# Optimization experiments

Hardware: AMD Instinct MI355X
Metric: run time of the kernel (lower is better)

Reference implementation:

```python
import jax, jax.numpy as jnp
import numpy as np

SCALE = 30.0
MARGIN = 0.4
H = 0.333
NUM_CLASSES = 100000
EMB = 512
BATCH = 512


def setup_inputs() -> dict:
    key = jax.random.key(0)
    k1, k2, k3 = jax.random.split(key, 3)
    embeddings = jax.random.normal(k1, (BATCH, EMB), dtype=jnp.float32)
    labels = jax.random.randint(k2, (BATCH,), 0, NUM_CLASSES, dtype=jnp.int64)
    # xavier_uniform: bound = sqrt(6 / (fan_in + fan_out)) with fan_in=EMB, fan_out=NUM_CLASSES
    bound = float(np.sqrt(6.0 / (EMB + NUM_CLASSES)))
    weight = jax.random.uniform(k3, (NUM_CLASSES, EMB), dtype=jnp.float32, minval=-bound, maxval=bound)
    return {"embeddings": embeddings, "labels": labels, "weight": weight}


def reference(embeddings, labels, weight):
    n = embeddings.shape[0]
    rows = jnp.arange(n)

    emb_norm = jnp.linalg.norm(embeddings, axis=1, keepdims=True)      # [N,1]
    w_unit = weight / jnp.linalg.norm(weight, axis=1, keepdims=True)   # [C,D]
    emb_unit = embeddings / emb_norm                                   # [N,D]
    cosine = emb_unit @ w_unit.T                                       # [N,C]

    batch_mean = jnp.mean(emb_norm)
    batch_std = jnp.std(emb_norm, ddof=1)  # torch.std is unbiased
    margin_scaler = jnp.clip((emb_norm - batch_mean) / (batch_std + H), -1.0, 1.0)  # [N,1]
    adaptive_margin = MARGIN * (1.0 + margin_scaler[:, 0])             # [N]

    # Apply angular margin only at the label position (equivalent to the
    # one_hot scatter + where in the original, without a second N x C pass).
    cos_t = cosine[rows, labels]                                       # [N]
    cos_t_m = jnp.cos(jnp.arccos(cos_t) + adaptive_margin)             # [N]
    logits = SCALE * cosine.at[rows, labels].set(cos_t_m)              # [N,C]

    # cross-entropy with mean reduction
    lse = jax.nn.logsumexp(logits, axis=1)                             # [N]
    loss = jnp.mean(lse - logits[rows, labels])
    return loss
```

## Files before the change

kernel.cpp:

```cpp
#include <hip/hip_runtime.h>
#include <hip/hip_bf16.h>

#define C_NUM 100000
#define D_EMB 512
#define N_BATCH 512
#define SCALE_F 30.0f
#define MARGIN_F 0.4f
#define H_F 0.333f
#define NT2 782
#define NCH 16

typedef __attribute__((ext_vector_type(8))) short bf16x8;
typedef __attribute__((ext_vector_type(4))) short bf16x4;
typedef __attribute__((ext_vector_type(4))) float f32x4;
typedef __attribute__((ext_vector_type(16))) float f32x16;

static __device__ __forceinline__ short f2bf(float f) {
  __hip_bfloat16 h = __float2bfloat16(f);
  union { __hip_bfloat16 b; short s; } u;
  u.b = h;
  return u.s;
}

static __device__ __forceinline__ float sq4(f32x4 v) {
  return v[0]*v[0] + v[1]*v[1] + v[2]*v[2] + v[3]*v[3];
}

static __device__ __forceinline__ void gload16(const void* g, void* l) {
  __builtin_amdgcn_global_load_lds(
      (const __attribute__((address_space(1))) void*)g,
      (__attribute__((address_space(3))) void*)l, 16, 0, 0);
}

__global__ __launch_bounds__(64) void k_rownorm(const float* __restrict__ emb,
                                                short* __restrict__ Aunit,
                                                float* __restrict__ norms) {
  const int i = blockIdx.x;
  const int l = threadIdx.x;
  const f32x4* row = reinterpret_cast<const f32x4*>(emb + (size_t)i * D_EMB);
  f32x4 v0 = row[l];
  f32x4 v1 = row[l + 64];
  float ss = sq4(v0) + sq4(v1);
#pragma unroll
  for (int m = 1; m < 64; m <<= 1) ss += __shfl_xor(ss, m);
  float nrm = sqrtf(ss);
  float inv = 1.0f / nrm;
  bf16x4 o0, o1;
#pragma unroll
  for (int q = 0; q < 4; ++q) { o0[q] = f2bf(v0[q] * inv); o1[q] = f2bf(v1[q] * inv); }
  bf16x4* dst = reinterpret_cast<bf16x4*>(Aunit + (size_t)i * D_EMB);
  dst[l] = o0;
  dst[l + 64] = o1;
  if (l == 0) norms[i] = nrm;
}

__global__ __launch_bounds__(512) void k_stats(const float* __restrict__ norms,
                                               float* __restrict__ marg) {
  __shared__ float red[8];
  const int t = threadIdx.x;
  const int lane = t & 63, wid = t >> 6;
  float x = norms[t];
  float s = x;
#pragma unroll
  for (int m = 1; m < 64; m <<= 1) s += __shfl_xor(s, m);
  if (lane == 0) red[wid] = s;
  __syncthreads();
  float tot = 0.f;
#pragma unroll
  for (int q = 0; q < 8; ++q) tot += red[q];
  const float mean = tot / 512.f;
  __syncthreads();
  float d = x - mean;
  float s2 = d * d;
#pragma unroll
  for (int m = 1; m < 64; m <<= 1) s2 += __shfl_xor(s2, m);
  if (lane == 0) red[wid] = s2;
  __syncthreads();
  float tot2 = 0.f;
#pragma unroll
  for (int q = 0; q < 8; ++q) tot2 += red[q];
  const float stdv = sqrtf(tot2 / 511.f);
  float msc = (x - mean) / (stdv + H_F);
  msc = fminf(1.f, fmaxf(-1.f, msc));
  marg[t] = MARGIN_F * (1.f + msc);
}

__global__ __launch_bounds__(256, 4) void k_main(const short* __restrict__ Aunit,
                                                 const float* __restrict__ weight,
                                                 const int* __restrict__ labels,
                                                 const float* __restrict__ marg,
                                                 float* __restrict__ partial,
                                                 float* __restrict__ tlogit) {
  __shared__ alignas(16) char As[2][8192];
  __shared__ alignas(16) char Ws[2][10240];
  __shared__ float winv[128];

  const int bid = blockIdx.x;
  const int grp = bid >> 5, within = bid & 31;
  const int rt = (within >> 3) & 3;
  const int ct = grp * 8 + (within & 7);
  if (ct >= NT2) return;

  const int tid = threadIdx.x;
  const int w = tid >> 6, lane = tid & 63;
  const int l31 = lane & 31, lhi = lane >> 5;

  const int ar0 = w * 32 + (lane >> 2);
  const int ak0 = ((lane & 3) * 16) ^ (((ar0 >> 1) & 3) << 4);
  const char* gA0 = (const char*)Aunit + (size_t)(rt * 128 + ar0) * 1024 + ak0;
  const char* gA1 = gA0 + (size_t)16 * 1024;

  const int sc8 = tid >> 3;
  const int su  = tid & 7;
  const float* wsrc[4];
  int wdst[4];
#pragma unroll
  for (int r = 0; r < 4; ++r) {
    int cls = r * 32 + sc8;
    int gcl = ct * 128 + cls; if (gcl > C_NUM - 1) gcl = C_NUM - 1;
    wsrc[r] = weight + (size_t)gcl * D_EMB + su * 4;
    wdst[r] = cls * 80 + su * 8;
  }

  const int xa = ((l31 >> 1) & 3) << 4;
  const int abase = (w * 32 + l31) * 64;

  f32x16 acc0, acc1, acc2, acc3;
#pragma unroll
  for (int q = 0; q < 16; ++q) { acc0[q] = 0.f; acc1[q] = 0.f; acc2[q] = 0.f; acc3[q] = 0.f; }
  float ssq0 = 0.f, ssq1 = 0.f, ssq2 = 0.f, ssq3 = 0.f;

  {
    gload16(gA0, &As[0][w * 2048]);
    gload16(gA1, &As[0][w * 2048 + 1024]);
    gA0 += 64; gA1 += 64;
    f32x4 v0 = *(const f32x4*)(wsrc[0]); wsrc[0] += 32;
    f32x4 v1 = *(const f32x4*)(wsrc[1]); wsrc[1] += 32;
    f32x4 v2 = *(const f32x4*)(wsrc[2]); wsrc[2] += 32;
    f32x4 v3 = *(const f32x4*)(wsrc[3]); wsrc[3] += 32;
    ssq0 += sq4(v0); ssq1 += sq4(v1); ssq2 += sq4(v2); ssq3 += sq4(v3);
    bf16x4 p0, p1, p2, p3;
#pragma unroll
    for (int e = 0; e < 4; ++e) { p0[e] = f2bf(v0[e]); p1[e] = f2bf(v1[e]);
                                  p2[e] = f2bf(v2[e]); p3[e] = f2bf(v3[e]); }
    *(bf16x4*)(&Ws[0][wdst[0]]) = p0;
    *(bf16x4*)(&Ws[0][wdst[1]]) = p1;
    *(bf16x4*)(&Ws[0][wdst[2]]) = p2;
    *(bf16x4*)(&Ws[0][wdst[3]]) = p3;
  }
  __syncthreads();

  int cur = 0;
  for (int c = 0; c < NCH; ++c) {
    const bool more = c < NCH - 1;
    f32x4 v0, v1, v2, v3;
    if (more) {
      gload16(gA0, &As[cur ^ 1][w * 2048]);
      gload16(gA1, &As[cur ^ 1][w * 2048 + 1024]);
      gA0 += 64; gA1 += 64;
      v0 = *(const f32x4*)(wsrc[0]); wsrc[0] += 32;
      v1 = *(const f32x4*)(wsrc[1]); wsrc[1] += 32;
      v2 = *(const f32x4*)(wsrc[2]); wsrc[2] += 32;
      v3 = *(const f32x4*)(wsrc[3]); wsrc[3] += 32;
    }

    const char* Ab = As[cur];
    const char* Wb = Ws[cur];
#pragma unroll
    for (int kk = 0; kk < 2; ++kk) {
      const int kb = kk * 32 + lhi * 16;
      bf16x8 a  = *(const bf16x8*)(Ab + abase + (kb ^ xa));
      bf16x8 b0 = *(const bf16x8*)(Wb + (l31)       * 80 + kb);
      bf16x8 b1 = *(const bf16x8*)(Wb + (32  + l31) * 80 + kb);
      bf16x8 b2 = *(const bf16x8*)(Wb + (64  + l31) * 80 + kb);
      bf16x8 b3 = *(const bf16x8*)(Wb + (96  + l31) * 80 + kb);
      acc0 = __builtin_amdgcn_mfma_f32_32x32x16_bf16(a, b0, acc0, 0, 0, 0);
      acc1 = __builtin_amdgcn_mfma_f32_32x32x16_bf16(a, b1, acc1, 0, 0, 0);
      acc2 = __builtin_amdgcn_mfma_f32_32x32x16_bf16(a, b2, acc2, 0, 0, 0);
      acc3 = __builtin_amdgcn_mfma_f32_32x32x16_bf16(a, b3, acc3, 0, 0, 0);
    }

    if (more) {
      ssq0 += sq4(v0); ssq1 += sq4(v1); ssq2 += sq4(v2); ssq3 += sq4(v3);
      bf16x4 p0, p1, p2, p3;
#pragma unroll
      for (int e = 0; e < 4; ++e) { p0[e] = f2bf(v0[e]); p1[e] = f2bf(v1[e]);
                                    p2[e] = f2bf(v2[e]); p3[e] = f2bf(v3[e]); }
      char* nb = (char*)Ws[cur ^ 1];
      *(bf16x4*)(nb + wdst[0]) = p0;
      *(bf16x4*)(nb + wdst[1]) = p1;
      *(bf16x4*)(nb + wdst[2]) = p2;
      *(bf16x4*)(nb + wdst[3]) = p3;
    }
    __syncthreads();
    cur ^= 1;
  }

  {
    float s0 = ssq0, s1 = ssq1, s2 = ssq2, s3 = ssq3;
#pragma unroll
    for (int m = 1; m < 8; m <<= 1) {
      s0 += __shfl_xor(s0, m); s1 += __shfl_xor(s1, m);
      s2 += __shfl_xor(s2, m); s3 += __shfl_xor(s3, m);
    }
    if (su == 0) {
      winv[sc8]      = (s0 > 0.f) ? rsqrtf(s0) : 0.f;
      winv[32 + sc8] = (s1 > 0.f) ? rsqrtf(s1) : 0.f;
      winv[64 + sc8] = (s2 > 0.f) ? rsqrtf(s2) : 0.f;
      winv[96 + sc8] = (s3 > 0.f) ? rsqrtf(s3) : 0.f;
    }
  }
  __syncthreads();

  const float wv0 = winv[l31];
  const float wv1 = winv[32 + l31];
  const float wv2 = winv[64 + l31];
  const float wv3 = winv[96 + l31];
  const int cb = ct * 128;
#pragma unroll
  for (int r = 0; r < 16; ++r) {
    const int rowf = (r & 3) + 8 * (r >> 2) + 4 * lhi;
    const int R = rt * 128 + w * 32 + rowf;
    const int lab = labels[R];
    float v = 0.f;
#pragma unroll
    for (int ni = 0; ni < 4; ++ni) {
      const int gcc = cb + ni * 32 + l31;
      const float wv = (ni == 0) ? wv0 : (ni == 1) ? wv1 : (ni == 2) ? wv2 : wv3;
      const float av = (ni == 0) ? acc0[r] : (ni == 1) ? acc1[r] : (ni == 2) ? acc2[r] : acc3[r];
      const float cosv = av * wv;
      float lg = SCALE_F * cosv;
      if (lab == gcc) {
        float ctv = fminf(1.f, fmaxf(-1.f, cosv));
        float lt = SCALE_F * cosf(acosf(ctv) + marg[R]);
        lg = lt;
        tlogit[R] = lt;
      }
      v += (gcc < C_NUM) ? __expf(lg) : 0.f;
    }
    v += __shfl_xor(v, 1);
    v += __shfl_xor(v, 2);
    v += __shfl_xor(v, 4);
    v += __shfl_xor(v, 8);
    v += __shfl_xor(v, 16);
    if (l31 == 0) partial[(size_t)ct * N_BATCH + R] = v;
  }
}

__global__ __launch_bounds__(64) void k_reduce(const float* __restrict__ partial,
                                               const float* __restrict__ tlogit,
                                               float* __restrict__ term) {
  const int r = blockIdx.x;
  const int l = threadIdx.x;
  float s = 0.f;
  for (int b = l; b < NT2; b += 64)
    s += partial[(size_t)b * N_BATCH + r];
#pragma unroll
  for (int m = 1; m < 64; m <<= 1) s += __shfl_xor(s, m);
  if (l == 0) term[r] = logf(s) - tlogit[r];
}

__global__ __launch_bounds__(512) void k_final(const float* __restrict__ term,
                                               float* __restrict__ out) {
  __shared__ float red[8];
  const int t = threadIdx.x;
  const int lane = t & 63, wid = t >> 6;
  float v = term[t];
#pragma unroll
  for (int m = 1; m < 64; m <<= 1) v += __shfl_xor(v, m);
  if (lane == 0) red[wid] = v;
  __syncthreads();
  if (t == 0) {
    float tot = 0.f;
#pragma unroll
    for (int q = 0; q < 8; ++q) tot += red[q];
    out[0] = tot / 512.f;
  }
}

extern "C" void kernel_launch(void* const* d_in, const int* in_sizes, int n_in,
                              void* d_out, int out_size, void* d_ws, size_t ws_size,
                              hipStream_t stream) {
  const float* emb    = (const float*)d_in[0];
  const int*   labels = (const int*)d_in[1];
  const float* weight = (const float*)d_in[2];
  float* out = (float*)d_out;

  char* ws = (char*)d_ws;
  short* Aunit   = (short*)ws;
  float* norms   = (float*)(ws + 524288);
  float* marg    = (float*)(ws + 524288 + 2048);
  float* tlog    = (float*)(ws + 524288 + 4096);
  float* term    = (float*)(ws + 524288 + 6144);
  float* partial = (float*)(ws + 524288 + 8192);

  k_rownorm<<<N_BATCH, 64, 0, stream>>>(emb, Aunit, norms);
  k_stats<<<1, 512, 0, stream>>>(norms, marg);
  k_main<<<98 * 32, 256, 0, stream>>>(Aunit, weight, labels, marg, partial, tlog);
  k_reduce<<<N_BATCH, 64, 0, stream>>>(partial, tlog, term);
  k_final<<<1, 512, 0, stream>>>(term, out);
}
```

Before: 137.5 us.

## Deepen weight prefetch to two chunks with explicit waitcnt and MFMA priority

Restructures the main GEMM loop into a manually unrolled ping-pong that keeps two chunks of fp32 weight loads in flight in registers, using explicit vmcnt/lgkmcnt waits and sched_barriers in place of compiler-managed scheduling. MFMA sections run at raised wave priority via s_setprio. The goal is to hide global weight-load latency behind the matrix math. The extra prefetch registers lead to lowering launch-bounds occupancy from 4 to 3 blocks per CU, which can reduce latency hiding across waves, and the hand-written waitcnt counts must exactly match the in-flight loads to stay correct.

```diff
diff --git a/kernel.cpp b/kernel.cpp
--- a/kernel.cpp
+++ b/kernel.cpp
@@ -85,7 +85,7 @@
   marg[t] = MARGIN_F * (1.f + msc);
 }
 
-__global__ __launch_bounds__(256, 4) void k_main(const short* __restrict__ Aunit,
+__global__ __launch_bounds__(256, 3) void k_main(const short* __restrict__ Aunit,
                                                  const float* __restrict__ weight,
                                                  const int* __restrict__ labels,
                                                  const float* __restrict__ marg,
@@ -107,19 +107,25 @@
 
   const int ar0 = w * 32 + (lane >> 2);
   const int ak0 = ((lane & 3) * 16) ^ (((ar0 >> 1) & 3) << 4);
-  const char* gA0 = (const char*)Aunit + (size_t)(rt * 128 + ar0) * 1024 + ak0;
-  const char* gA1 = gA0 + (size_t)16 * 1024;
+  const char* gAb0 = (const char*)Aunit + (size_t)(rt * 128 + ar0) * 1024 + ak0;
+  const char* gAb1 = gAb0 + (size_t)16 * 1024;
 
   const int sc8 = tid >> 3;
   const int su  = tid & 7;
-  const float* wsrc[4];
-  int wdst[4];
-#pragma unroll
-  for (int r = 0; r < 4; ++r) {
-    int cls = r * 32 + sc8;
-    int gcl = ct * 128 + cls; if (gcl > C_NUM - 1) gcl = C_NUM - 1;
-    wsrc[r] = weight + (size_t)gcl * D_EMB + su * 4;
-    wdst[r] = cls * 80 + su * 8;
+  const float* wbase0; const float* wbase1; const float* wbase2; const float* wbase3;
+  int wdst0, wdst1, wdst2, wdst3;
+  {
+    int c0 = 0 * 32 + sc8, c1 = 1 * 32 + sc8, c2 = 2 * 32 + sc8, c3 = 3 * 32 + sc8;
+    int g0 = ct * 128 + c0; if (g0 > C_NUM - 1) g0 = C_NUM - 1;
+    int g1 = ct * 128 + c1; if (g1 > C_NUM - 1) g1 = C_NUM - 1;
+    int g2 = ct * 128 + c2; if (g2 > C_NUM - 1) g2 = C_NUM - 1;
+    int g3 = ct * 128 + c3; if (g3 > C_NUM - 1) g3 = C_NUM - 1;
+    wbase0 = weight + (size_t)g0 * D_EMB + su * 4;
+    wbase1 = weight + (size_t)g1 * D_EMB + su * 4;
+    wbase2 = weight + (size_t)g2 * D_EMB + su * 4;
+    wbase3 = weight + (size_t)g3 * D_EMB + su * 4;
+    wdst0 = c0 * 80 + su * 8; wdst1 = c1 * 80 + su * 8;
+    wdst2 = c2 * 80 + su * 8; wdst3 = c3 * 80 + su * 8;
   }
 
   const int xa = ((l31 >> 1) & 3) << 4;
@@ -130,70 +136,90 @@
   for (int q = 0; q < 16; ++q) { acc0[q] = 0.f; acc1[q] = 0.f; acc2[q] = 0.f; acc3[q] = 0.f; }
   float ssq0 = 0.f, ssq1 = 0.f, ssq2 = 0.f, ssq3 = 0.f;
 
-  {
-    gload16(gA0, &As[0][w * 2048]);
-    gload16(gA1, &As[0][w * 2048 + 1024]);
-    gA0 += 64; gA1 += 64;
-    f32x4 v0 = *(const f32x4*)(wsrc[0]); wsrc[0] += 32;
-    f32x4 v1 = *(const f32x4*)(wsrc[1]); wsrc[1] += 32;
-    f32x4 v2 = *(const f32x4*)(wsrc[2]); wsrc[2] += 32;
-    f32x4 v3 = *(const f32x4*)(wsrc[3]); wsrc[3] += 32;
-    ssq0 += sq4(v0); ssq1 += sq4(v1); ssq2 += sq4(v2); ssq3 += sq4(v3);
-    bf16x4 p0, p1, p2, p3;
-#pragma unroll
-    for (int e = 0; e < 4; ++e) { p0[e] = f2bf(v0[e]); p1[e] = f2bf(v1[e]);
-                                  p2[e] = f2bf(v2[e]); p3[e] = f2bf(v3[e]); }
-    *(bf16x4*)(&Ws[0][wdst[0]]) = p0;
-    *(bf16x4*)(&Ws[0][wdst[1]]) = p1;
-    *(bf16x4*)(&Ws[0][wdst[2]]) = p2;
-    *(bf16x4*)(&Ws[0][wdst[3]]) = p3;
-  }
-  __syncthreads();
-
-  int cur = 0;
-  for (int c = 0; c < NCH; ++c) {
-    const bool more = c < NCH - 1;
-    f32x4 v0, v1, v2, v3;
-    if (more) {
-      gload16(gA0, &As[cur ^ 1][w * 2048]);
-      gload16(gA1, &As[cur ^ 1][w * 2048 + 1024]);
-      gA0 += 64; gA1 += 64;
-      v0 = *(const f32x4*)(wsrc[0]); wsrc[0] += 32;
-      v1 = *(const f32x4*)(wsrc[1]); wsrc[1] += 32;
-      v2 = *(const f32x4*)(wsrc[2]); wsrc[2] += 32;
-      v3 = *(const f32x4*)(wsrc[3]); wsrc[3] += 32;
-    }
-
-    const char* Ab = As[cur];
-    const char* Wb = Ws[cur];
-#pragma unroll
-    for (int kk = 0; kk < 2; ++kk) {
-      const int kb = kk * 32 + lhi * 16;
-      bf16x8 a  = *(const bf16x8*)(Ab + abase + (kb ^ xa));
-      bf16x8 b0 = *(const bf16x8*)(Wb + (l31)       * 80 + kb);
-      bf16x8 b1 = *(const bf16x8*)(Wb + (32  + l31) * 80 + kb);
-      bf16x8 b2 = *(const bf16x8*)(Wb + (64  + l31) * 80 + kb);
-      bf16x8 b3 = *(const bf16x8*)(Wb + (96  + l31) * 80 + kb);
-      acc0 = __builtin_amdgcn_mfma_f32_32x32x16_bf16(a, b0, acc0, 0, 0, 0);
-      acc1 = __builtin_amdgcn_mfma_f32_32x32x16_bf16(a, b1, acc1, 0, 0, 0);
-      acc2 = __builtin_amdgcn_mfma_f32_32x32x16_bf16(a, b2, acc2, 0, 0, 0);
-      acc3 = __builtin_amdgcn_mfma_f32_32x32x16_bf16(a, b3, acc3, 0, 0, 0);
-    }
-
-    if (more) {
-      ssq0 += sq4(v0); ssq1 += sq4(v1); ssq2 += sq4(v2); ssq3 += sq4(v3);
-      bf16x4 p0, p1, p2, p3;
-#pragma unroll
-      for (int e = 0; e < 4; ++e) { p0[e] = f2bf(v0[e]); p1[e] = f2bf(v1[e]);
-                                    p2[e] = f2bf(v2[e]); p3[e] = f2bf(v3[e]); }
-      char* nb = (char*)Ws[cur ^ 1];
-      *(bf16x4*)(nb + wdst[0]) = p0;
-      *(bf16x4*)(nb + wdst[1]) = p1;
-      *(bf16x4*)(nb + wdst[2]) = p2;
-      *(bf16x4*)(nb + wdst[3]) = p3;
-    }
-    __syncthreads();
-    cur ^= 1;
+  f32x4 pa0, pa1, pa2, pa3;
+  f32x4 pb0, pb1, pb2, pb3;
+
+#define WLOAD(R0,R1,R2,R3,OFF) { \
+    R0 = *(const f32x4*)(wbase0 + (OFF)); R1 = *(const f32x4*)(wbase1 + (OFF)); \
+    R2 = *(const f32x4*)(wbase2 + (OFF)); R3 = *(const f32x4*)(wbase3 + (OFF)); }
+
+#define WWRITE(BUF,R0,R1,R2,R3) { \
+    bf16x4 t0, t1, t2, t3; \
+    _Pragma("unroll") \
+    for (int e = 0; e < 4; ++e) { t0[e] = f2bf(R0[e]); t1[e] = f2bf(R1[e]); \
+                                  t2[e] = f2bf(R2[e]); t3[e] = f2bf(R3[e]); } \
+    *(bf16x4*)(&Ws[BUF][wdst0]) = t0; *(bf16x4*)(&Ws[BUF][wdst1]) = t1; \
+    *(bf16x4*)(&Ws[BUF][wdst2]) = t2; *(bf16x4*)(&Ws[BUF][wdst3]) = t3; }
+
+#define SSQADD(R0,R1,R2,R3) { ssq0 += sq4(R0); ssq1 += sq4(R1); \
+                              ssq2 += sq4(R2); ssq3 += sq4(R3); }
+
+#define COMPUTE(BUF) { \
+    const char* Ab = As[BUF]; const char* Wb = Ws[BUF]; \
+    __builtin_amdgcn_s_setprio(1); \
+    _Pragma("unroll") \
+    for (int kk = 0; kk < 2; ++kk) { \
+      const int kb = kk * 32 + lhi * 16; \
+      bf16x8 a  = *(const bf16x8*)(Ab + abase + (kb ^ xa)); \
+      bf16x8 b0 = *(const bf16x8*)(Wb + (l31)      * 80 + kb); \
+      bf16x8 b1 = *(const bf16x8*)(Wb + (32 + l31) * 80 + kb); \
+      bf16x8 b2 = *(const bf16x8*)(Wb + (64 + l31) * 80 + kb); \
+      bf16x8 b3 = *(const bf16x8*)(Wb + (96 + l31) * 80 + kb); \
+      acc0 = __builtin_amdgcn_mfma_f32_32x32x16_bf16(a, b0, acc0, 0, 0, 0); \
+      acc1 = __builtin_amdgcn_mfma_f32_32x32x16_bf16(a, b1, acc1, 0, 0, 0); \
+      acc2 = __builtin_amdgcn_mfma_f32_32x32x16_bf16(a, b2, acc2, 0, 0, 0); \
+      acc3 = __builtin_amdgcn_mfma_f32_32x32x16_bf16(a, b3, acc3, 0, 0, 0); \
+    } \
+    __builtin_amdgcn_s_setprio(0); }
+
+  WLOAD(pa0, pa1, pa2, pa3, 0);
+  __builtin_amdgcn_sched_barrier(0);
+  gload16(gAb0, &As[0][w * 2048]);
+  gload16(gAb1, &As[0][w * 2048 + 1024]);
+  __builtin_amdgcn_sched_barrier(0);
+  WLOAD(pb0, pb1, pb2, pb3, 32);
+  __builtin_amdgcn_sched_barrier(0);
+  asm volatile("s_waitcnt vmcnt(4)" ::: "memory");
+  SSQADD(pa0, pa1, pa2, pa3);
+  WWRITE(0, pa0, pa1, pa2, pa3);
+  asm volatile("s_waitcnt lgkmcnt(0)" ::: "memory");
+  __builtin_amdgcn_s_barrier();
+  __builtin_amdgcn_sched_barrier(0);
+
+  for (int i = 0; i < 8; ++i) {
+    {
+      const int ao = (2 * i + 1) * 64;
+      gload16(gAb0 + ao, &As[1][w * 2048]);
+      gload16(gAb1 + ao, &As[1][w * 2048 + 1024]);
+      __builtin_amdgcn_sched_barrier(0);
+      int cw = 2 * i + 2; if (cw > 15) cw = 15;
+      WLOAD(pa0, pa1, pa2, pa3, cw * 32);
+      __builtin_amdgcn_sched_barrier(0);
+      COMPUTE(0);
+      asm volatile("s_waitcnt vmcnt(4)" ::: "memory");
+      SSQADD(pb0, pb1, pb2, pb3);
+      WWRITE(1, pb0, pb1, pb2, pb3);
+      asm volatile("s_waitcnt lgkmcnt(0)" ::: "memory");
+      __builtin_amdgcn_s_barrier();
+      __builtin_amdgcn_sched_barrier(0);
+    }
+    {
+      int ca = 2 * i + 2; if (ca > 15) ca = 15;
+      const int ao = ca * 64;
+      gload16(gAb0 + ao, &As[0][w * 2048]);
+      gload16(gAb1 + ao, &As[0][w * 2048 + 1024]);
+      __builtin_amdgcn_sched_barrier(0);
+      int cw = 2 * i + 3; if (cw > 15) cw = 15;
+      WLOAD(pb0, pb1, pb2, pb3, cw * 32);
+      __builtin_amdgcn_sched_barrier(0);
+      COMPUTE(1);
+      asm volatile("s_waitcnt vmcnt(4)" ::: "memory");
+      if (2 * i + 2 <= 15) SSQADD(pa0, pa1, pa2, pa3);
+      WWRITE(0, pa0, pa1, pa2, pa3);
+      asm volatile("s_waitcnt lgkmcnt(0)" ::: "memory");
+      __builtin_amdgcn_s_barrier();
+      __builtin_amdgcn_sched_barrier(0);
+    }
   }
 
   {
@@ -245,6 +271,10 @@
     v += __shfl_xor(v, 16);
     if (l31 == 0) partial[(size_t)ct * N_BATCH + R] = v;
   }
+#undef WLOAD
+#undef WWRITE
+#undef SSQADD
+#undef COMPUTE
 }
 
 __global__ __launch_bounds__(64) void k_reduce(const float* __restrict__ partial,
```

New measurement: 134.6 us. 2.1% less time.

## Stage whole A tile in LDS and give each wave private W slices

Applied to the files above, without the earlier changes.

The main kernel now loads the block's full 128x512 bf16 embedding tile into 128KB of LDS once, instead of double-buffering 64-wide K chunks. Each wave independently streams its own 32 weight classes through a private LDS slice, with four register-prefetched stages, so the per-chunk block barriers are removed. Partial sums are first reduced across waves in LDS and written row-major with a padded stride, so the reduce kernel reads contiguously. The 128KB LDS footprint limits occupancy to one block per CU. Global-load latency must now be hidden by register prefetching rather than by multiple resident blocks.

```diff
diff --git a/kernel.cpp b/kernel.cpp
--- a/kernel.cpp
+++ b/kernel.cpp
@@ -8,7 +8,7 @@
 #define MARGIN_F 0.4f
 #define H_F 0.333f
 #define NT2 782
-#define NCH 16
+#define PST 784
 
 typedef __attribute__((ext_vector_type(8))) short bf16x8;
 typedef __attribute__((ext_vector_type(4))) short bf16x4;
@@ -85,15 +85,16 @@
   marg[t] = MARGIN_F * (1.f + msc);
 }
 
-__global__ __launch_bounds__(256, 4) void k_main(const short* __restrict__ Aunit,
-                                                 const float* __restrict__ weight,
-                                                 const int* __restrict__ labels,
-                                                 const float* __restrict__ marg,
-                                                 float* __restrict__ partial,
-                                                 float* __restrict__ tlogit) {
-  __shared__ alignas(16) char As[2][8192];
-  __shared__ alignas(16) char Ws[2][10240];
-  __shared__ float winv[128];
+__global__ __launch_bounds__(256) void k_main(const short* __restrict__ Aunit,
+                                              const float* __restrict__ weight,
+                                              const int* __restrict__ labels,
+                                              const float* __restrict__ marg,
+                                              float* __restrict__ partial,
+                                              float* __restrict__ tlogit) {
+  __shared__ alignas(16) char Astat[131072];
+  __shared__ alignas(16) char Wsl[4][2816];
+  __shared__ float winv[4][32];
+  __shared__ float rowsum[128][4];
 
   const int bid = blockIdx.x;
   const int grp = bid >> 5, within = bid & 31;
@@ -104,147 +105,153 @@
   const int tid = threadIdx.x;
   const int w = tid >> 6, lane = tid & 63;
   const int l31 = lane & 31, lhi = lane >> 5;
-
-  const int ar0 = w * 32 + (lane >> 2);
-  const int ak0 = ((lane & 3) * 16) ^ (((ar0 >> 1) & 3) << 4);
-  const char* gA0 = (const char*)Aunit + (size_t)(rt * 128 + ar0) * 1024 + ak0;
-  const char* gA1 = gA0 + (size_t)16 * 1024;
-
-  const int sc8 = tid >> 3;
-  const int su  = tid & 7;
-  const float* wsrc[4];
-  int wdst[4];
-#pragma unroll
-  for (int r = 0; r < 4; ++r) {
-    int cls = r * 32 + sc8;
-    int gcl = ct * 128 + cls; if (gcl > C_NUM - 1) gcl = C_NUM - 1;
-    wsrc[r] = weight + (size_t)gcl * D_EMB + su * 4;
-    wdst[r] = cls * 80 + su * 8;
-  }
-
-  const int xa = ((l31 >> 1) & 3) << 4;
-  const int abase = (w * 32 + l31) * 64;
+  const int lhi16 = lhi * 16;
+  const int xr = (l31 & 15) << 4;
+
+  {
+    const char* Asrc = (const char*)Aunit + (size_t)(rt * 128 + w * 32) * 1024;
+    char* Adst = &Astat[(w * 32) * 1024];
+    const int ls = lane * 16;
+#pragma unroll
+    for (int i = 0; i < 32; ++i)
+      gload16(Asrc + (size_t)i * 1024 + (ls ^ ((i & 15) << 4)), Adst + i * 1024);
+  }
+  __builtin_amdgcn_sched_barrier(0);
+
+  const int su = lane & 7;
+  const int c8 = lane >> 3;
+  const float* wb0; const float* wb1; const float* wb2; const float* wb3;
+  int wd0, wd1, wd2, wd3;
+  {
+    int l0 = w * 32 + 0 * 8 + c8, l1 = w * 32 + 1 * 8 + c8;
+    int l2 = w * 32 + 2 * 8 + c8, l3 = w * 32 + 3 * 8 + c8;
+    int g0 = ct * 128 + l0; if (g0 > C_NUM - 1) g0 = C_NUM - 1;
+    int g1 = ct * 128 + l1; if (g1 > C_NUM - 1) g1 = C_NUM - 1;
+    int g2 = ct * 128 + l2; if (g2 > C_NUM - 1) g2 = C_NUM - 1;
+    int g3 = ct * 128 + l3; if (g3 > C_NUM - 1) g3 = C_NUM - 1;
+    wb0 = weight + (size_t)g0 * D_EMB + su * 4;
+    wb1 = weight + (size_t)g1 * D_EMB + su * 4;
+    wb2 = weight + (size_t)g2 * D_EMB + su * 4;
+    wb3 = weight + (size_t)g3 * D_EMB + su * 4;
+    wd0 = (0 * 8 + c8) * 88 + su * 8; wd1 = (1 * 8 + c8) * 88 + su * 8;
+    wd2 = (2 * 8 + c8) * 88 + su * 8; wd3 = (3 * 8 + c8) * 88 + su * 8;
+  }
+  char* Wme = &Wsl[w][0];
+  const int bb = l31 * 88 + lhi16;
+
+  const int ab0 = (0 * 32 + l31) * 1024;
+  const int ab1 = (1 * 32 + l31) * 1024;
+  const int ab2 = (2 * 32 + l31) * 1024;
+  const int ab3 = (3 * 32 + l31) * 1024;
 
   f32x16 acc0, acc1, acc2, acc3;
 #pragma unroll
   for (int q = 0; q < 16; ++q) { acc0[q] = 0.f; acc1[q] = 0.f; acc2[q] = 0.f; acc3[q] = 0.f; }
-  float ssq0 = 0.f, ssq1 = 0.f, ssq2 = 0.f, ssq3 = 0.f;
+  float sq0 = 0.f, sq1 = 0.f, sq2 = 0.f, sq3 = 0.f;
+
+  f32x4 pA0, pA1, pA2, pA3;
+  f32x4 pB0, pB1, pB2, pB3;
+  f32x4 pC0, pC1, pC2, pC3;
+  f32x4 pD0, pD1, pD2, pD3;
+
+#define WLOADSET(S0,S1,S2,S3,OFF) { \
+    S0 = *(const f32x4*)(wb0 + (OFF)); S1 = *(const f32x4*)(wb1 + (OFF)); \
+    S2 = *(const f32x4*)(wb2 + (OFF)); S3 = *(const f32x4*)(wb3 + (OFF)); }
+
+#define PHASE(S0,S1,S2,S3,C) { \
+    sq0 += sq4(S0); sq1 += sq4(S1); sq2 += sq4(S2); sq3 += sq4(S3); \
+    { bf16x4 t0, t1, t2, t3; \
+      _Pragma("unroll") \
+      for (int e = 0; e < 4; ++e) { t0[e] = f2bf(S0[e]); t1[e] = f2bf(S1[e]); \
+                                    t2[e] = f2bf(S2[e]); t3[e] = f2bf(S3[e]); } \
+      *(bf16x4*)(Wme + wd0) = t0; *(bf16x4*)(Wme + wd1) = t1; \
+      *(bf16x4*)(Wme + wd2) = t2; *(bf16x4*)(Wme + wd3) = t3; } \
+    asm volatile("s_waitcnt lgkmcnt(0)" ::: "memory"); \
+    __builtin_amdgcn_sched_barrier(0); \
+    { int nc = (C) + 4; if (nc > 15) nc = 15; \
+      WLOADSET(S0, S1, S2, S3, nc * 32); } \
+    _Pragma("unroll") \
+    for (int kk = 0; kk < 2; ++kk) { \
+      const int ka = (((C) * 64 + kk * 32 + lhi16) ^ xr); \
+      bf16x8 a0 = *(const bf16x8*)(Astat + ab0 + ka); \
+      bf16x8 a1 = *(const bf16x8*)(Astat + ab1 + ka); \
+      bf16x8 a2 = *(const bf16x8*)(Astat + ab2 + ka); \
+      bf16x8 a3 = *(const bf16x8*)(Astat + ab3 + ka); \
+      bf16x8 b  = *(const bf16x8*)(Wme + bb + kk * 32); \
+      acc0 = __builtin_amdgcn_mfma_f32_32x32x16_bf16(a0, b, acc0, 0, 0, 0); \
+      acc1 = __builtin_amdgcn_mfma_f32_32x32x16_bf16(a1, b, acc1, 0, 0, 0); \
+      acc2 = __builtin_amdgcn_mfma_f32_32x32x16_bf16(a2, b, acc2, 0, 0, 0); \
+      acc3 = __builtin_amdgcn_mfma_f32_32x32x16_bf16(a3, b, acc3, 0, 0, 0); \
+    } }
+
+  WLOADSET(pA0, pA1, pA2, pA3, 0);
+  WLOADSET(pB0, pB1, pB2, pB3, 32);
+  WLOADSET(pC0, pC1, pC2, pC3, 64);
+  WLOADSET(pD0, pD1, pD2, pD3, 96);
+  __builtin_amdgcn_sched_barrier(0);
+  asm volatile("s_waitcnt vmcnt(16)" ::: "memory");
+  __builtin_amdgcn_s_barrier();
+  __builtin_amdgcn_sched_barrier(0);
+
+#pragma unroll
+  for (int i = 0; i < 4; ++i) {
+    PHASE(pA0, pA1, pA2, pA3, 4 * i + 0);
+    PHASE(pB0, pB1, pB2, pB3, 4 * i + 1);
+    PHASE(pC0, pC1, pC2, pC3, 4 * i + 2);
+    PHASE(pD0, pD1, pD2, pD3, 4 * i + 3);
+  }
 
   {
-    gload16(gA0, &As[0][w * 2048]);
-    gload16(gA1, &As[0][w * 2048 + 1024]);
-    gA0 += 64; gA1 += 64;
-    f32x4 v0 = *(const f32x4*)(wsrc[0]); wsrc[0] += 32;
-    f32x4 v1 = *(const f32x4*)(wsrc[1]); wsrc[1] += 32;
-    f32x4 v2 = *(const f32x4*)(wsrc[2]); wsrc[2] += 32;
-    f32x4 v3 = *(const f32x4*)(wsrc[3]); wsrc[3] += 32;
-    ssq0 += sq4(v0); ssq1 += sq4(v1); ssq2 += sq4(v2); ssq3 += sq4(v3);
-    bf16x4 p0, p1, p2, p3;
-#pragma unroll
-    for (int e = 0; e < 4; ++e) { p0[e] = f2bf(v0[e]); p1[e] = f2bf(v1[e]);
-                                  p2[e] = f2bf(v2[e]); p3[e] = f2bf(v3[e]); }
-    *(bf16x4*)(&Ws[0][wdst[0]]) = p0;
-    *(bf16x4*)(&Ws[0][wdst[1]]) = p1;
-    *(bf16x4*)(&Ws[0][wdst[2]]) = p2;
-    *(bf16x4*)(&Ws[0][wdst[3]]) = p3;
-  }
-  __syncthreads();
-
-  int cur = 0;
-  for (int c = 0; c < NCH; ++c) {
-    const bool more = c < NCH - 1;
-    f32x4 v0, v1, v2, v3;
-    if (more) {
-      gload16(gA0, &As[cur ^ 1][w * 2048]);
-      gload16(gA1, &As[cur ^ 1][w * 2048 + 1024]);
-      gA0 += 64; gA1 += 64;
-      v0 = *(const f32x4*)(wsrc[0]); wsrc[0] += 32;
-      v1 = *(const f32x4*)(wsrc[1]); wsrc[1] += 32;
-      v2 = *(const f32x4*)(wsrc[2]); wsrc[2] += 32;
-      v3 = *(const f32x4*)(wsrc[3]); wsrc[3] += 32;
-    }
-
-    const char* Ab = As[cur];
-    const char* Wb = Ws[cur];
-#pragma unroll
-    for (int kk = 0; kk < 2; ++kk) {
-      const int kb = kk * 32 + lhi * 16;
-      bf16x8 a  = *(const bf16x8*)(Ab + abase + (kb ^ xa));
-      bf16x8 b0 = *(const bf16x8*)(Wb + (l31)       * 80 + kb);
-      bf16x8 b1 = *(const bf16x8*)(Wb + (32  + l31) * 80 + kb);
-      bf16x8 b2 = *(const bf16x8*)(Wb + (64  + l31) * 80 + kb);
-      bf16x8 b3 = *(const bf16x8*)(Wb + (96  + l31) * 80 + kb);
-      acc0 = __builtin_amdgcn_mfma_f32_32x32x16_bf16(a, b0, acc0, 0, 0, 0);
-      acc1 = __builtin_amdgcn_mfma_f32_32x32x16_bf16(a, b1, acc1, 0, 0, 0);
-      acc2 = __builtin_amdgcn_mfma_f32_32x32x16_bf16(a, b2, acc2, 0, 0, 0);
-      acc3 = __builtin_amdgcn_mfma_f32_32x32x16_bf16(a, b3, acc3, 0, 0, 0);
-    }
-
-    if (more) {
-      ssq0 += sq4(v0); ssq1 += sq4(v1); ssq2 += sq4(v2); ssq3 += sq4(v3);
-      bf16x4 p0, p1, p2, p3;
-#pragma unroll
-      for (int e = 0; e < 4; ++e) { p0[e] = f2bf(v0[e]); p1[e] = f2bf(v1[e]);
-                                    p2[e] = f2bf(v2[e]); p3[e] = f2bf(v3[e]); }
-      char* nb = (char*)Ws[cur ^ 1];
-      *(bf16x4*)(nb + wdst[0]) = p0;
-      *(bf16x4*)(nb + wdst[1]) = p1;
-      *(bf16x4*)(nb + wdst[2]) = p2;
-      *(bf16x4*)(nb + wdst[3]) = p3;
-    }
-    __syncthreads();
-    cur ^= 1;
-  }
-
-  {
-    float s0 = ssq0, s1 = ssq1, s2 = ssq2, s3 = ssq3;
+    float s0 = sq0, s1 = sq1, s2 = sq2, s3 = sq3;
 #pragma unroll
     for (int m = 1; m < 8; m <<= 1) {
       s0 += __shfl_xor(s0, m); s1 += __shfl_xor(s1, m);
       s2 += __shfl_xor(s2, m); s3 += __shfl_xor(s3, m);
     }
     if (su == 0) {
-      winv[sc8]      = (s0 > 0.f) ? rsqrtf(s0) : 0.f;
-      winv[32 + sc8] = (s1 > 0.f) ? rsqrtf(s1) : 0.f;
-      winv[64 + sc8] = (s2 > 0.f) ? rsqrtf(s2) : 0.f;
-      winv[96 + sc8] = (s3 > 0.f) ? rsqrtf(s3) : 0.f;
+      winv[w][0 * 8 + c8]  = (s0 > 0.f) ? rsqrtf(s0) : 0.f;
+      winv[w][1 * 8 + c8]  = (s1 > 0.f) ? rsqrtf(s1) : 0.f;
+      winv[w][2 * 8 + c8]  = (s2 > 0.f) ? rsqrtf(s2) : 0.f;
+      winv[w][3 * 8 + c8]  = (s3 > 0.f) ? rsqrtf(s3) : 0.f;
     }
   }
-  __syncthreads();
-
-  const float wv0 = winv[l31];
-  const float wv1 = winv[32 + l31];
-  const float wv2 = winv[64 + l31];
-  const float wv3 = winv[96 + l31];
-  const int cb = ct * 128;
-#pragma unroll
-  for (int r = 0; r < 16; ++r) {
-    const int rowf = (r & 3) + 8 * (r >> 2) + 4 * lhi;
-    const int R = rt * 128 + w * 32 + rowf;
-    const int lab = labels[R];
-    float v = 0.f;
-#pragma unroll
-    for (int ni = 0; ni < 4; ++ni) {
-      const int gcc = cb + ni * 32 + l31;
-      const float wv = (ni == 0) ? wv0 : (ni == 1) ? wv1 : (ni == 2) ? wv2 : wv3;
-      const float av = (ni == 0) ? acc0[r] : (ni == 1) ? acc1[r] : (ni == 2) ? acc2[r] : acc3[r];
+  asm volatile("s_waitcnt lgkmcnt(0)" ::: "memory");
+  __builtin_amdgcn_sched_barrier(0);
+  const float wv = winv[w][l31];
+
+  const int gcc = ct * 128 + w * 32 + l31;
+  const bool ok = gcc < C_NUM;
+#pragma unroll
+  for (int mi = 0; mi < 4; ++mi) {
+#pragma unroll
+    for (int r = 0; r < 16; ++r) {
+      const int rowf = (r & 3) + 8 * (r >> 2) + 4 * lhi;
+      const int rloc = mi * 32 + rowf;
+      const int R = rt * 128 + rloc;
+      const float av = (mi == 0) ? acc0[r] : (mi == 1) ? acc1[r] : (mi == 2) ? acc2[r] : acc3[r];
       const float cosv = av * wv;
       float lg = SCALE_F * cosv;
-      if (lab == gcc) {
+      if (labels[R] == gcc) {
         float ctv = fminf(1.f, fmaxf(-1.f, cosv));
         float lt = SCALE_F * cosf(acosf(ctv) + marg[R]);
         lg = lt;
         tlogit[R] = lt;
       }
-      v += (gcc < C_NUM) ? __expf(lg) : 0.f;
+      float v = ok ? __expf(lg) : 0.f;
+      v += __shfl_xor(v, 1);
+      v += __shfl_xor(v, 2);
+      v += __shfl_xor(v, 4);
+      v += __shfl_xor(v, 8);
+      v += __shfl_xor(v, 16);
+      if (l31 == 0) rowsum[rloc][w] = v;
     }
-    v += __shfl_xor(v, 1);
-    v += __shfl_xor(v, 2);
-    v += __shfl_xor(v, 4);
-    v += __shfl_xor(v, 8);
-    v += __shfl_xor(v, 16);
-    if (l31 == 0) partial[(size_t)ct * N_BATCH + R] = v;
-  }
+  }
+  __syncthreads();
+  if (tid < 128)
+    partial[(size_t)(rt * 128 + tid) * PST + ct] =
+        (rowsum[tid][0] + rowsum[tid][1]) + (rowsum[tid][2] + rowsum[tid][3]);
+#undef WLOADSET
+#undef PHASE
 }
 
 __global__ __launch_bounds__(64) void k_reduce(const float* __restrict__ partial,
@@ -252,9 +259,10 @@
                                                float* __restrict__ term) {
   const int r = blockIdx.x;
   const int l = threadIdx.x;
+  const float* row = partial + (size_t)r * PST;
   float s = 0.f;
   for (int b = l; b < NT2; b += 64)
-    s += partial[(size_t)b * N_BATCH + r];
+    s += row[b];
 #pragma unroll
   for (int m = 1; m < 64; m <<= 1) s += __shfl_xor(s, m);
   if (l == 0) term[r] = logf(s) - tlogit[r];
```

Result: slower. 363.0 us (+163.9%).
